# Kernel tuning notes

Hardware: AMD Instinct MI355X
Metric: run time of the kernel (lower is better)

The kernel has to match this reference:

```python
import jax, jax.numpy as jnp
import numpy as np

EPS = 1e-5
NUM_GN_GROUPS = 32


def setup_inputs() -> dict:
    key = jax.random.key(0)
    k1, k2, k3 = jax.random.split(key, 3)
    B, C, N, G = 2, 256, 4096, 8
    c = C // G
    return {
        "points": jax.random.normal(k1, (B, C, N), dtype=jnp.float32),
        "conv_w": jax.random.normal(k2, (G, c, c), dtype=jnp.float32) / np.sqrt(c),
        "conv_b": jax.random.normal(k3, (C,), dtype=jnp.float32) * 0.02,
        "gn_w": jnp.ones((C,), dtype=jnp.float32),
        "gn_b": jnp.zeros((C,), dtype=jnp.float32),
    }


def reference(points, conv_w, conv_b, gn_w, gn_b):
    B, C, N = points.shape
    G = conv_w.shape[0]
    c = C // G  # channels per attention group
    identity = points

    # grouped 1x1 conv: per-group [c,c] matmul + bias
    x = points.reshape(B, G, c, N)
    x = jnp.einsum('gij,bgjn->bgin', conv_w, x) + conv_b.reshape(1, G, c, 1)

    # attention[b,g,n,m] = sum_i x[b,g,i,n] * x[b,g,i,m] / sqrt(c)
    scale = 1.0 / np.sqrt(c).astype(np.float32)
    attn = jnp.einsum('bgin,bgim->bgnm', x, x) * scale
    # softmax over dim=2 (the query/row N axis -- non-standard)
    attn = jax.nn.softmax(attn, axis=2)

    # ELU-gated second matmul: [B,G,c,N] @ [B,G,N,N] -> [B,G,c,N]
    x = jnp.einsum('bgcn,bgnm->bgcm', jax.nn.elu(x), attn)

    # channel shuffle: [B,G,c,N] -> [B,c,G,N] -> [B,C,N]
    x = x.transpose(0, 2, 1, 3).reshape(B, C, N)
    x = x + identity

    # GroupNorm(32 groups) over (channels-in-group, N)
    xg = x.reshape(B, NUM_GN_GROUPS, C // NUM_GN_GROUPS, N)
    mean = xg.mean(axis=(2, 3), keepdims=True)
    var = xg.var(axis=(2, 3), keepdims=True)
    xg = (xg - mean) * jax.lax.rsqrt(var + EPS)
    x = xg.reshape(B, C, N)
    return x * gn_w.reshape(1, C, 1) + gn_b.reshape(1, C, 1)
```

## Files before the change

### kernel.cpp

```cpp
#include <hip/hip_runtime.h>

typedef __attribute__((ext_vector_type(8))) short bf16x8;
typedef __attribute__((ext_vector_type(4))) short bf16x4;
typedef __attribute__((ext_vector_type(4))) float f32x4;

#if __has_builtin(__builtin_amdgcn_exp2f)
#define EXP2(x) __builtin_amdgcn_exp2f(x)
#else
#define EXP2(x) exp2f(x)
#endif

__device__ __forceinline__ unsigned short f2bf(float f) {
    union { float f; unsigned int u; } v; v.f = f;
    unsigned int r = v.u + 0x7fffu + ((v.u >> 16) & 1u);
    return (unsigned short)(r >> 16);
}

__device__ __forceinline__ float asf(unsigned int u) {
    union { unsigned int u; float f; } v; v.u = u; return v.f;
}

#define QK_PRESCALE 0.50500983f

__global__ __launch_bounds__(256) void conv_kernel(
    const float* __restrict__ points, const float* __restrict__ conv_w,
    const float* __restrict__ conv_b,
    unsigned short* __restrict__ xqT, unsigned short* __restrict__ xv)
{
    __shared__ float w[1024];
    const int h  = blockIdx.x >> 6;
    const int nc = blockIdx.x & 63;
    const int g  = h & 7;
    const int tid = threadIdx.x;
    const float* wg = conv_w + g * 1024;
    for (int k = tid; k < 1024; k += 256) w[k] = wg[k];
    __syncthreads();
    const int n  = nc * 64 + (tid & 63);
    const int ig = tid >> 6;
    const float* p = points + (size_t)h * 32 * 4096 + n;
    float pv[32];
#pragma unroll
    for (int j = 0; j < 32; ++j) pv[j] = p[(size_t)j * 4096];
    float out[8];
#pragma unroll
    for (int ii = 0; ii < 8; ++ii) {
        const int i = ig * 8 + ii;
        float acc = conv_b[g * 32 + i];
        const float4* w4 = (const float4*)(w + i * 32);
#pragma unroll
        for (int j4 = 0; j4 < 8; ++j4) {
            float4 ww = w4[j4];
            acc += ww.x * pv[j4 * 4]     + ww.y * pv[j4 * 4 + 1]
                 + ww.z * pv[j4 * 4 + 2] + ww.w * pv[j4 * 4 + 3];
        }
        out[ii] = acc;
    }
    unsigned short tq[8];
#pragma unroll
    for (int ii = 0; ii < 8; ++ii) tq[ii] = f2bf(out[ii] * QK_PRESCALE);
    *(bf16x8*)(xqT + ((size_t)h * 4096 + n) * 32 + ig * 8) = *(bf16x8*)tq;
#pragma unroll
    for (int ii = 0; ii < 8; ++ii) {
        float x = out[ii];
        float e = x > 0.f ? x : (__expf(x) - 1.f);
        xv[((size_t)h * 32 + ig * 8 + ii) * 4096 + n] = f2bf(e);
    }
}

#define VSTR 136
#define PSTR 72

#if __has_builtin(__builtin_amdgcn_cvt_pk_bf16_f32)
typedef __attribute__((ext_vector_type(2))) __bf16 bf16x2v;
__device__ __forceinline__ bf16x4 exp_pack(f32x4 sc, float& lsum) {
    float e0 = EXP2(sc[0]), e1 = EXP2(sc[1]);
    float e2 = EXP2(sc[2]), e3 = EXP2(sc[3]);
    lsum += (e0 + e1) + (e2 + e3);
    union { bf16x2v v[2]; bf16x4 s; } u;
    u.v[0] = __builtin_amdgcn_cvt_pk_bf16_f32(e0, e1);
    u.v[1] = __builtin_amdgcn_cvt_pk_bf16_f32(e2, e3);
    return u.s;
}
#else
__device__ __forceinline__ bf16x4 exp_pack(f32x4 sc, float& lsum) {
    union { float f; unsigned int u; } e0, e1, e2, e3;
    e0.f = EXP2(sc[0]); e1.f = EXP2(sc[1]); e2.f = EXP2(sc[2]); e3.f = EXP2(sc[3]);
    unsigned int t0 = e0.u & 0xffff0000u, t1 = e1.u & 0xffff0000u;
    unsigned int t2 = e2.u & 0xffff0000u, t3 = e3.u & 0xffff0000u;
    lsum += (asf(t0) + asf(t1)) + (asf(t2) + asf(t3));
    union { unsigned int d[2]; bf16x4 v; } pk;
    pk.d[0] = (t0 >> 16) | t1;
    pk.d[1] = (t2 >> 16) | t3;
    return pk.v;
}
#endif

#define CHUNK(C0, KU, KP)                                                      \
    {                                                                          \
        __syncthreads();                                                       \
        *(bf16x8*)(Vt + vi * VSTR + vn)      = va;                             \
        *(bf16x8*)(Vt + vi * VSTR + vn + 64) = vb;                             \
        __syncthreads();                                                       \
        const int pfb = ((C0) + 128) & 4095;                                   \
        va = *(const bf16x8*)(vbase + (size_t)vi * 4096 + pfb + vn);           \
        vb = *(const bf16x8*)(vbase + (size_t)vi * 4096 + pfb + vn + 64);      \
        _Pragma("unroll")                                                      \
        for (int s8 = 0; s8 < 8; ++s8)                                         \
            KP[s8] = *(const bf16x8*)(kfp + (size_t)(pfb + s8 * 16) * 32);     \
        _Pragma("unroll")                                                      \
        for (int sub = 0; sub < 2; ++sub) {                                    \
            _Pragma("unroll")                                                  \
            for (int s = 0; s < 4; ++s) {                                      \
                f32x4 sc = __builtin_amdgcn_mfma_f32_16x16x32_bf16(            \
                    KU[sub * 4 + s], qfrag, (f32x4){0.f, 0.f, 0.f, 0.f},       \
                    0, 0, 0);                                                  \
                bf16x4 pk = exp_pack(sc, lsum);                                \
                *(bf16x4*)(pw + l15 * PSTR + s * 16 + quad * 4) = pk;          \
            }                                                                  \
            _Pragma("unroll")                                                  \
            for (int ng = 0; ng < 2; ++ng) {                                   \
                bf16x8 pfrag = *(const bf16x8*)(pw + l15 * PSTR + ng * 32 +    \
                                                quad * 8);                     \
                const int col = sub * 64 + ng * 32 + quad * 8;                 \
                bf16x8 v0 = *(const bf16x8*)(Vt + l15 * VSTR + col);           \
                bf16x8 v1 = *(const bf16x8*)(Vt + (16 + l15) * VSTR + col);    \
                acc0 = __builtin_amdgcn_mfma_f32_16x16x32_bf16(v0, pfrag,      \
                                                               acc0, 0, 0, 0); \
                acc1 = __builtin_amdgcn_mfma_f32_16x16x32_bf16(v1, pfrag,      \
                                                               acc1, 0, 0, 0); \
            }                                                                  \
        }                                                                      \
    }

__global__ __launch_bounds__(256, 4) void attn_kernel(
    const unsigned short* __restrict__ xqT,
    const unsigned short* __restrict__ xv,
    const float* __restrict__ points,
    float* __restrict__ z)
{
    __shared__ unsigned short Vt[32 * VSTR];
    __shared__ unsigned short Pl[4][16 * PSTR];

    const int h  = blockIdx.y;
    const int b = h >> 3, g = h & 7;
    const int tid = threadIdx.x;
    const int wv = tid >> 6, lane = tid & 63;
    const int quad = lane >> 4, l15 = lane & 15;

    const int m = blockIdx.x * 64 + wv * 16 + l15;

    const unsigned short* kbase = xqT + (size_t)h * 4096 * 32;
    const unsigned short* vbase = xv  + (size_t)h * 32 * 4096;

    const bf16x8 qfrag = *(const bf16x8*)(kbase + (size_t)m * 32 + quad * 8);

    f32x4 acc0 = {0.f, 0.f, 0.f, 0.f};
    f32x4 acc1 = {0.f, 0.f, 0.f, 0.f};
    float lsum = 0.f;

    const int vi = tid >> 3, vn = (tid & 7) * 8;
    unsigned short* pw = &Pl[wv][0];

    const unsigned short* kfp = kbase + (size_t)l15 * 32 + quad * 8;

    const unsigned short* vptr = vbase + (size_t)vi * 4096 + vn;
    bf16x8 va = *(const bf16x8*)vptr;
    bf16x8 vb = *(const bf16x8*)(vptr + 64);

    bf16x8 kA[8], kB[8];
#pragma unroll
    for (int s8 = 0; s8 < 8; ++s8)
        kA[s8] = *(const bf16x8*)(kfp + (size_t)(s8 * 16) * 32);

    for (int n0 = 0; n0 < 4096; n0 += 256) {
        CHUNK(n0,       kA, kB);
        CHUNK(n0 + 128, kB, kA);
    }

    lsum += __shfl_xor(lsum, 16, 64);
    lsum += __shfl_xor(lsum, 32, 64);
    const float inv = 1.f / lsum;

    const float* pb = points + (size_t)b * 256 * 4096;
    float* zb = z + (size_t)b * 256 * 4096;
#pragma unroll
    for (int half = 0; half < 2; ++half) {
        f32x4 a = half ? acc1 : acc0;
#pragma unroll
        for (int r = 0; r < 4; ++r) {
            int i = half * 16 + quad * 4 + r;
            size_t off = (size_t)(i * 8 + g) * 4096 + m;
            zb[off] = a[r] * inv + pb[off];
        }
    }
}

__global__ __launch_bounds__(256) void gn_stats(const float* __restrict__ z,
                                                float* __restrict__ pstats)
{
    const int blk = blockIdx.x;
    const int tid = threadIdx.x;
    const float4* p = (const float4*)(z + (size_t)blk * 8192);
    float s = 0.f, ss = 0.f;
    for (int k = tid; k < 2048; k += 256) {
        float4 v = p[k];
        s  += v.x + v.y + v.z + v.w;
        ss += v.x * v.x + v.y * v.y + v.z * v.z + v.w * v.w;
    }
#pragma unroll
    for (int off = 32; off > 0; off >>= 1) {
        s  += __shfl_down(s, off, 64);
        ss += __shfl_down(ss, off, 64);
    }
    __shared__ float red[8];
    const int w = tid >> 6;
    if ((tid & 63) == 0) { red[w * 2] = s; red[w * 2 + 1] = ss; }
    __syncthreads();
    if (tid == 0) {
        s  = red[0] + red[2] + red[4] + red[6];
        ss = red[1] + red[3] + red[5] + red[7];
        pstats[blk * 2]     = s;
        pstats[blk * 2 + 1] = ss;
    }
}

__global__ __launch_bounds__(256) void gn_apply(float* __restrict__ z,
                                                const float* __restrict__ pstats,
                                                const float* __restrict__ gw,
                                                const float* __restrict__ gb)
{
    const int idx = blockIdx.x * 256 + threadIdx.x;
    float4* p = (float4*)z;
    float4 v = p[idx];
    const int chg = idx >> 10;
    const int grp = chg >> 3;
    const int ch  = chg & 255;
    const float4 s4  = *(const float4*)(pstats + grp * 8);
    const float4 s4b = *(const float4*)(pstats + grp * 8 + 4);
    const float s  = s4.x + s4.z + s4b.x + s4b.z;
    const float ss = s4.y + s4.w + s4b.y + s4b.w;
    const float mean = s * (1.f / 32768.f);
    const float var  = ss * (1.f / 32768.f) - mean * mean;
    const float rstd = rsqrtf(var + 1e-5f);
    const float w  = gw[ch] * rstd;
    const float bb = gb[ch] - mean * w;
    v.x = v.x * w + bb; v.y = v.y * w + bb;
    v.z = v.z * w + bb; v.w = v.w * w + bb;
    p[idx] = v;
}

extern "C" void kernel_launch(void* const* d_in, const int* in_sizes, int n_in,
                              void* d_out, int out_size, void* d_ws, size_t ws_size,
                              hipStream_t stream)
{
    const float* points = (const float*)d_in[0];
    const float* conv_w = (const float*)d_in[1];
    const float* conv_b = (const float*)d_in[2];
    const float* gn_w   = (const float*)d_in[3];
    const float* gn_b   = (const float*)d_in[4];
    float* out = (float*)d_out;
    char* ws = (char*)d_ws;
    unsigned short* xqT = (unsigned short*)ws;
    unsigned short* xv  = (unsigned short*)(ws + (size_t)4 * 1024 * 1024);
    float* pstats = (float*)(ws + (size_t)8 * 1024 * 1024);

    conv_kernel<<<1024, 256, 0, stream>>>(points, conv_w, conv_b, xqT, xv);
    attn_kernel<<<dim3(64, 16), 256, 0, stream>>>(xqT, xv, points, out);
    gn_stats<<<256, 256, 0, stream>>>(out, pstats);
    gn_apply<<<2048, 256, 0, stream>>>(out, pstats, gn_w, gn_b);
}
```

Baseline: 152.9 us.

## Double-buffer V tile, fuse GroupNorm partial stats into attention epilogue, remap blocks

The V tile in LDS is now double-buffered, so each chunk needs one barrier instead of two, and V is prefetched two chunks ahead. The attention epilogue computes per-wave partial sums and sums of squares of its outputs and writes them to a workspace. A small combine kernel then reduces these into mean and rstd, replacing the stats kernel that re-read the full output. The grid is flattened and remapped so that neighbouring blocks handle different heads, which may change L2 locality, at the cost of more LDS per block, extra shuffles in the epilogue, and more register pressure.

```diff
diff --git a/kernel.cpp b/kernel.cpp
--- a/kernel.cpp
+++ b/kernel.cpp
@@ -95,18 +95,18 @@
 }
 #endif
 
-#define CHUNK(C0, KU, KP)                                                      \
+#define CHUNK(C0, KU, KP, VCUR, VNXT)                                          \
     {                                                                          \
         __syncthreads();                                                       \
-        *(bf16x8*)(Vt + vi * VSTR + vn)      = va;                             \
-        *(bf16x8*)(Vt + vi * VSTR + vn + 64) = vb;                             \
-        __syncthreads();                                                       \
-        const int pfb = ((C0) + 128) & 4095;                                   \
-        va = *(const bf16x8*)(vbase + (size_t)vi * 4096 + pfb + vn);           \
-        vb = *(const bf16x8*)(vbase + (size_t)vi * 4096 + pfb + vn + 64);      \
+        *(bf16x8*)((VNXT) + vi * VSTR + vn)      = va;                         \
+        *(bf16x8*)((VNXT) + vi * VSTR + vn + 64) = vb;                         \
+        const int pf1 = ((C0) + 128) & 4095;                                   \
+        const int pf2 = ((C0) + 256) & 4095;                                   \
+        va = *(const bf16x8*)(vbase + (size_t)vi * 4096 + pf2 + vn);           \
+        vb = *(const bf16x8*)(vbase + (size_t)vi * 4096 + pf2 + vn + 64);      \
         _Pragma("unroll")                                                      \
         for (int s8 = 0; s8 < 8; ++s8)                                         \
-            KP[s8] = *(const bf16x8*)(kfp + (size_t)(pfb + s8 * 16) * 32);     \
+            KP[s8] = *(const bf16x8*)(kfp + (size_t)(pf1 + s8 * 16) * 32);     \
         _Pragma("unroll")                                                      \
         for (int sub = 0; sub < 2; ++sub) {                                    \
             _Pragma("unroll")                                                  \
@@ -122,8 +122,8 @@
                 bf16x8 pfrag = *(const bf16x8*)(pw + l15 * PSTR + ng * 32 +    \
                                                 quad * 8);                     \
                 const int col = sub * 64 + ng * 32 + quad * 8;                 \
-                bf16x8 v0 = *(const bf16x8*)(Vt + l15 * VSTR + col);           \
-                bf16x8 v1 = *(const bf16x8*)(Vt + (16 + l15) * VSTR + col);    \
+                bf16x8 v0 = *(const bf16x8*)((VCUR) + l15 * VSTR + col);       \
+                bf16x8 v1 = *(const bf16x8*)((VCUR) + (16 + l15) * VSTR + col);\
                 acc0 = __builtin_amdgcn_mfma_f32_16x16x32_bf16(v0, pfrag,      \
                                                                acc0, 0, 0, 0); \
                 acc1 = __builtin_amdgcn_mfma_f32_16x16x32_bf16(v1, pfrag,      \
@@ -136,18 +136,21 @@
     const unsigned short* __restrict__ xqT,
     const unsigned short* __restrict__ xv,
     const float* __restrict__ points,
-    float* __restrict__ z)
-{
-    __shared__ unsigned short Vt[32 * VSTR];
+    float* __restrict__ z, float* __restrict__ pstats)
+{
+    __shared__ unsigned short Vt0[32 * VSTR];
+    __shared__ unsigned short Vt1[32 * VSTR];
     __shared__ unsigned short Pl[4][16 * PSTR];
 
-    const int h  = blockIdx.y;
+    const int bid = blockIdx.x;
+    const int h  = (bid & 7) * 2 + ((bid >> 3) & 1);
+    const int qt = bid >> 4;
     const int b = h >> 3, g = h & 7;
     const int tid = threadIdx.x;
     const int wv = tid >> 6, lane = tid & 63;
     const int quad = lane >> 4, l15 = lane & 15;
 
-    const int m = blockIdx.x * 64 + wv * 16 + l15;
+    const int m = qt * 64 + wv * 16 + l15;
 
     const unsigned short* kbase = xqT + (size_t)h * 4096 * 32;
     const unsigned short* vbase = xv  + (size_t)h * 32 * 4096;
@@ -163,18 +166,22 @@
 
     const unsigned short* kfp = kbase + (size_t)l15 * 32 + quad * 8;
 
-    const unsigned short* vptr = vbase + (size_t)vi * 4096 + vn;
-    bf16x8 va = *(const bf16x8*)vptr;
-    bf16x8 vb = *(const bf16x8*)(vptr + 64);
-
+    {
+        bf16x8 t0 = *(const bf16x8*)(vbase + (size_t)vi * 4096 + vn);
+        bf16x8 t1 = *(const bf16x8*)(vbase + (size_t)vi * 4096 + vn + 64);
+        *(bf16x8*)(Vt0 + vi * VSTR + vn)      = t0;
+        *(bf16x8*)(Vt0 + vi * VSTR + vn + 64) = t1;
+    }
+    bf16x8 va = *(const bf16x8*)(vbase + (size_t)vi * 4096 + 128 + vn);
+    bf16x8 vb = *(const bf16x8*)(vbase + (size_t)vi * 4096 + 128 + vn + 64);
     bf16x8 kA[8], kB[8];
 #pragma unroll
     for (int s8 = 0; s8 < 8; ++s8)
         kA[s8] = *(const bf16x8*)(kfp + (size_t)(s8 * 16) * 32);
 
     for (int n0 = 0; n0 < 4096; n0 += 256) {
-        CHUNK(n0,       kA, kB);
-        CHUNK(n0 + 128, kB, kA);
+        CHUNK(n0,       kA, kB, Vt0, Vt1);
+        CHUNK(n0 + 128, kB, kA, Vt1, Vt0);
     }
 
     lsum += __shfl_xor(lsum, 16, 64);
@@ -183,29 +190,43 @@
 
     const float* pb = points + (size_t)b * 256 * 4096;
     float* zb = z + (size_t)b * 256 * 4096;
+    float* sb = pstats + ((size_t)bid * 4 + wv) * 64;
+
 #pragma unroll
     for (int half = 0; half < 2; ++half) {
         f32x4 a = half ? acc1 : acc0;
 #pragma unroll
         for (int r = 0; r < 4; ++r) {
-            int i = half * 16 + quad * 4 + r;
-            size_t off = (size_t)(i * 8 + g) * 4096 + m;
-            zb[off] = a[r] * inv + pb[off];
+            const int i = half * 16 + quad * 4 + r;
+            const size_t off = (size_t)(i * 8 + g) * 4096;
+            float zA = a[r] * inv + pb[off + m];
+            zb[off + m] = zA;
+            float s  = zA;
+            float ss = zA * zA;
+            s += __shfl_xor(s, 1, 64);  ss += __shfl_xor(ss, 1, 64);
+            s += __shfl_xor(s, 2, 64);  ss += __shfl_xor(ss, 2, 64);
+            s += __shfl_xor(s, 4, 64);  ss += __shfl_xor(ss, 4, 64);
+            s += __shfl_xor(s, 8, 64);  ss += __shfl_xor(ss, 8, 64);
+            if (l15 == 0) {
+                sb[i * 2]     = s;
+                sb[i * 2 + 1] = ss;
+            }
         }
     }
 }
 
-__global__ __launch_bounds__(256) void gn_stats(const float* __restrict__ z,
-                                                float* __restrict__ pstats)
-{
-    const int blk = blockIdx.x;
+__global__ __launch_bounds__(256) void gn_combine(const float* __restrict__ pstats,
+                                                  float* __restrict__ stats)
+{
+    const int b = blockIdx.x >> 5;
+    const int i = blockIdx.x & 31;
     const int tid = threadIdx.x;
-    const float4* p = (const float4*)(z + (size_t)blk * 8192);
     float s = 0.f, ss = 0.f;
     for (int k = tid; k < 2048; k += 256) {
-        float4 v = p[k];
-        s  += v.x + v.y + v.z + v.w;
-        ss += v.x * v.x + v.y * v.y + v.z * v.z + v.w * v.w;
+        const int wvk = k & 3, j = k >> 2;
+        const int bid = (j & 3) | (b << 2) | ((j >> 2) << 3);
+        const float* p = pstats + ((size_t)bid * 4 + wvk) * 64 + i * 2;
+        s += p[0]; ss += p[1];
     }
 #pragma unroll
     for (int off = 32; off > 0; off >>= 1) {
@@ -219,13 +240,15 @@
     if (tid == 0) {
         s  = red[0] + red[2] + red[4] + red[6];
         ss = red[1] + red[3] + red[5] + red[7];
-        pstats[blk * 2]     = s;
-        pstats[blk * 2 + 1] = ss;
+        float mean = s * (1.f / 32768.f);
+        float var  = ss * (1.f / 32768.f) - mean * mean;
+        stats[blockIdx.x * 2]     = mean;
+        stats[blockIdx.x * 2 + 1] = rsqrtf(var + 1e-5f);
     }
 }
 
 __global__ __launch_bounds__(256) void gn_apply(float* __restrict__ z,
-                                                const float* __restrict__ pstats,
+                                                const float* __restrict__ stats,
                                                 const float* __restrict__ gw,
                                                 const float* __restrict__ gb)
 {
@@ -233,15 +256,9 @@
     float4* p = (float4*)z;
     float4 v = p[idx];
     const int chg = idx >> 10;
-    const int grp = chg >> 3;
+    const int blk = chg >> 3;
     const int ch  = chg & 255;
-    const float4 s4  = *(const float4*)(pstats + grp * 8);
-    const float4 s4b = *(const float4*)(pstats + grp * 8 + 4);
-    const float s  = s4.x + s4.z + s4b.x + s4b.z;
-    const float ss = s4.y + s4.w + s4b.y + s4b.w;
-    const float mean = s * (1.f / 32768.f);
-    const float var  = ss * (1.f / 32768.f) - mean * mean;
-    const float rstd = rsqrtf(var + 1e-5f);
+    const float mean = stats[blk * 2], rstd = stats[blk * 2 + 1];
     const float w  = gw[ch] * rstd;
     const float bb = gb[ch] - mean * w;
     v.x = v.x * w + bb; v.y = v.y * w + bb;
@@ -263,9 +280,10 @@
     unsigned short* xqT = (unsigned short*)ws;
     unsigned short* xv  = (unsigned short*)(ws + (size_t)4 * 1024 * 1024);
     float* pstats = (float*)(ws + (size_t)8 * 1024 * 1024);
+    float* stats  = (float*)(ws + (size_t)9 * 1024 * 1024);
 
     conv_kernel<<<1024, 256, 0, stream>>>(points, conv_w, conv_b, xqT, xv);
-    attn_kernel<<<dim3(64, 16), 256, 0, stream>>>(xqT, xv, points, out);
-    gn_stats<<<256, 256, 0, stream>>>(out, pstats);
-    gn_apply<<<2048, 256, 0, stream>>>(out, pstats, gn_w, gn_b);
-}
+    attn_kernel<<<1024, 256, 0, stream>>>(xqT, xv, points, out, pstats);
+    gn_combine<<<64, 256, 0, stream>>>(pstats, stats);
+    gn_apply<<<2048, 256, 0, stream>>>(out, stats, gn_w, gn_b);
+}
```

Measured after the change: 158.0 us. 1.03x slower.

## Fuse GroupNorm statistics into attention epilogue and drop gn_stats kernel

Applied to the files above, without the earlier changes.

The attention kernel now computes per-wave partial sums and sums of squares of its output rows and writes them to a workspace. The separate stats kernel that re-read the whole output is removed. gn_apply reduces the partials per block before normalizing. This removes one full pass over the output and one launch, at the cost of a redundant partial reduction in every apply block and extra shuffles in the attention epilogue.

```diff
diff --git a/kernel.cpp b/kernel.cpp
--- a/kernel.cpp
+++ b/kernel.cpp
@@ -136,18 +136,19 @@
     const unsigned short* __restrict__ xqT,
     const unsigned short* __restrict__ xv,
     const float* __restrict__ points,
-    float* __restrict__ z)
+    float* __restrict__ z, float* __restrict__ pstats)
 {
     __shared__ unsigned short Vt[32 * VSTR];
     __shared__ unsigned short Pl[4][16 * PSTR];
 
+    const int qt = blockIdx.x;
     const int h  = blockIdx.y;
     const int b = h >> 3, g = h & 7;
     const int tid = threadIdx.x;
     const int wv = tid >> 6, lane = tid & 63;
     const int quad = lane >> 4, l15 = lane & 15;
 
-    const int m = blockIdx.x * 64 + wv * 16 + l15;
+    const int m = qt * 64 + wv * 16 + l15;
 
     const unsigned short* kbase = xqT + (size_t)h * 4096 * 32;
     const unsigned short* vbase = xv  + (size_t)h * 32 * 4096;
@@ -163,9 +164,8 @@
 
     const unsigned short* kfp = kbase + (size_t)l15 * 32 + quad * 8;
 
-    const unsigned short* vptr = vbase + (size_t)vi * 4096 + vn;
-    bf16x8 va = *(const bf16x8*)vptr;
-    bf16x8 vb = *(const bf16x8*)(vptr + 64);
+    bf16x8 va = *(const bf16x8*)(vbase + (size_t)vi * 4096 + vn);
+    bf16x8 vb = *(const bf16x8*)(vbase + (size_t)vi * 4096 + vn + 64);
 
     bf16x8 kA[8], kB[8];
 #pragma unroll
@@ -183,29 +183,47 @@
 
     const float* pb = points + (size_t)b * 256 * 4096;
     float* zb = z + (size_t)b * 256 * 4096;
+    float* sb = pstats + (((size_t)h * 64 + qt) * 4 + wv) * 64;
+
 #pragma unroll
     for (int half = 0; half < 2; ++half) {
         f32x4 a = half ? acc1 : acc0;
 #pragma unroll
         for (int r = 0; r < 4; ++r) {
-            int i = half * 16 + quad * 4 + r;
-            size_t off = (size_t)(i * 8 + g) * 4096 + m;
-            zb[off] = a[r] * inv + pb[off];
+            const int i = half * 16 + quad * 4 + r;
+            const size_t off = (size_t)(i * 8 + g) * 4096;
+            float zA = a[r] * inv + pb[off + m];
+            zb[off + m] = zA;
+            float s  = zA;
+            float ss = zA * zA;
+            s += __shfl_xor(s, 1, 64);  ss += __shfl_xor(ss, 1, 64);
+            s += __shfl_xor(s, 2, 64);  ss += __shfl_xor(ss, 2, 64);
+            s += __shfl_xor(s, 4, 64);  ss += __shfl_xor(ss, 4, 64);
+            s += __shfl_xor(s, 8, 64);  ss += __shfl_xor(ss, 8, 64);
+            if (l15 == 0) {
+                sb[i * 2]     = s;
+                sb[i * 2 + 1] = ss;
+            }
         }
     }
 }
 
-__global__ __launch_bounds__(256) void gn_stats(const float* __restrict__ z,
-                                                float* __restrict__ pstats)
-{
-    const int blk = blockIdx.x;
+__global__ __launch_bounds__(256) void gn_apply(float* __restrict__ z,
+                                                const float* __restrict__ pstats,
+                                                const float* __restrict__ gw,
+                                                const float* __restrict__ gb)
+{
+    const int chg = blockIdx.x >> 2;
+    const int b = chg >> 8, ch = chg & 255;
+    const int i = ch >> 3;
     const int tid = threadIdx.x;
-    const float4* p = (const float4*)(z + (size_t)blk * 8192);
+
     float s = 0.f, ss = 0.f;
     for (int k = tid; k < 2048; k += 256) {
-        float4 v = p[k];
-        s  += v.x + v.y + v.z + v.w;
-        ss += v.x * v.x + v.y * v.y + v.z * v.z + v.w * v.w;
+        const int hloc = k >> 8, rest = k & 255;
+        const float* p = pstats +
+            (((size_t)(b * 8 + hloc) * 64) * 4 + rest) * 64 + i * 2;
+        s += p[0]; ss += p[1];
     }
 #pragma unroll
     for (int off = 32; off > 0; off >>= 1) {
@@ -213,40 +231,29 @@
         ss += __shfl_down(ss, off, 64);
     }
     __shared__ float red[8];
+    __shared__ float mrs[2];
     const int w = tid >> 6;
     if ((tid & 63) == 0) { red[w * 2] = s; red[w * 2 + 1] = ss; }
     __syncthreads();
     if (tid == 0) {
         s  = red[0] + red[2] + red[4] + red[6];
         ss = red[1] + red[3] + red[5] + red[7];
-        pstats[blk * 2]     = s;
-        pstats[blk * 2 + 1] = ss;
-    }
-}
-
-__global__ __launch_bounds__(256) void gn_apply(float* __restrict__ z,
-                                                const float* __restrict__ pstats,
-                                                const float* __restrict__ gw,
-                                                const float* __restrict__ gb)
-{
-    const int idx = blockIdx.x * 256 + threadIdx.x;
-    float4* p = (float4*)z;
-    float4 v = p[idx];
-    const int chg = idx >> 10;
-    const int grp = chg >> 3;
-    const int ch  = chg & 255;
-    const float4 s4  = *(const float4*)(pstats + grp * 8);
-    const float4 s4b = *(const float4*)(pstats + grp * 8 + 4);
-    const float s  = s4.x + s4.z + s4b.x + s4b.z;
-    const float ss = s4.y + s4.w + s4b.y + s4b.w;
-    const float mean = s * (1.f / 32768.f);
-    const float var  = ss * (1.f / 32768.f) - mean * mean;
-    const float rstd = rsqrtf(var + 1e-5f);
-    const float w  = gw[ch] * rstd;
-    const float bb = gb[ch] - mean * w;
-    v.x = v.x * w + bb; v.y = v.y * w + bb;
-    v.z = v.z * w + bb; v.w = v.w * w + bb;
-    p[idx] = v;
+        float mean = s * (1.f / 32768.f);
+        float var  = ss * (1.f / 32768.f) - mean * mean;
+        mrs[0] = mean;
+        mrs[1] = rsqrtf(var + 1e-5f);
+    }
+    __syncthreads();
+    const float mean = mrs[0], rstd = mrs[1];
+    const float wgt = gw[ch] * rstd;
+    const float bb  = gb[ch] - mean * wgt;
+
+    const int idx = blockIdx.x * 256 + tid;
+    float4* p4 = (float4*)z;
+    float4 v = p4[idx];
+    v.x = v.x * wgt + bb; v.y = v.y * wgt + bb;
+    v.z = v.z * wgt + bb; v.w = v.w * wgt + bb;
+    p4[idx] = v;
 }
 
 extern "C" void kernel_launch(void* const* d_in, const int* in_sizes, int n_in,
@@ -260,12 +267,12 @@
     const float* gn_b   = (const float*)d_in[4];
     float* out = (float*)d_out;
     char* ws = (char*)d_ws;
+    const size_t MB = 1024 * 1024;
     unsigned short* xqT = (unsigned short*)ws;
-    unsigned short* xv  = (unsigned short*)(ws + (size_t)4 * 1024 * 1024);
-    float* pstats = (float*)(ws + (size_t)8 * 1024 * 1024);
+    unsigned short* xv  = (unsigned short*)(ws + 4 * MB);
+    float* pstats = (float*)(ws + 8 * MB);
 
     conv_kernel<<<1024, 256, 0, stream>>>(points, conv_w, conv_b, xqT, xv);
-    attn_kernel<<<dim3(64, 16), 256, 0, stream>>>(xqT, xv, points, out);
-    gn_stats<<<256, 256, 0, stream>>>(out, pstats);
+    attn_kernel<<<dim3(64, 16), 256, 0, stream>>>(xqT, xv, points, out, pstats);
     gn_apply<<<2048, 256, 0, stream>>>(out, pstats, gn_w, gn_b);
 }
```

New measurement: 164.0 us. 1.07x slower.
